# Kernel tuning notes

Measured on AMD Instinct MI355X. Metric: run time of the kernel, lower is better.

## Reference

```python
import jax, jax.numpy as jnp
import numpy as np

B, T, D = 8, 2048, 512
KQ, K = 32, 4  # DemandRouter defaults: k_query=32, k_topk=4


def setup_inputs() -> dict:
    key = jax.random.key(0)
    ks = jax.random.split(key, 9)

    def init(k, shape, fan_in):
        return (jax.random.normal(k, shape, jnp.float32) / np.sqrt(fan_in)).astype(jnp.float32)

    return dict(
        x=jax.random.normal(ks[0], (B, T, D), jnp.float32),
        # DemandRouter projections
        Wq=init(ks[1], (D, KQ), D), bq=jnp.zeros((KQ,), jnp.float32),
        Wk=init(ks[2], (D, KQ), D), bk=jnp.zeros((KQ,), jnp.float32),
        # System1 FFN (D -> 2D -> D) + LayerNorm
        W1=init(ks[3], (D, 2 * D), D), b1=jnp.zeros((2 * D,), jnp.float32),
        W2=init(ks[4], (2 * D, D), 2 * D), b2=jnp.zeros((D,), jnp.float32),
        ln_g=jnp.ones((D,), jnp.float32), ln_b=jnp.zeros((D,), jnp.float32),
        # System2 transform (2D -> 2D -> D)
        Wt1=init(ks[5], (2 * D, 2 * D), 2 * D), bt1=jnp.zeros((2 * D,), jnp.float32),
        Wt2=init(ks[6], (2 * D, D), 2 * D), bt2=jnp.zeros((D,), jnp.float32),
        # output projection
        Wo=init(ks[7], (D, D), D), bo=jnp.zeros((D,), jnp.float32),
    )


def reference(x, Wq, bq, Wk, bk, W1, b1, W2, b2, ln_g, ln_b, Wt1, bt1, Wt2, bt2, Wo, bo):
    # ---- DemandRouter: topk over query-key similarity, gather neighbors, mean ----
    q = x @ Wq + bq                      # [B,T,KQ]
    k = x @ Wk + bk                      # [B,T,KQ]
    sim = jnp.einsum('btk,bsk->bts', q, k) / np.float32(np.sqrt(KQ))  # [B,T,T]
    _, idx = jax.lax.top_k(sim, K)       # [B,T,K]
    # gather x[b, idx[b,t]] and mean over K neighbors -> [B,T,D]
    gathered = jax.vmap(lambda xb, ib: xb[ib])(x, idx).mean(axis=2)

    # ---- System1: residual FFN (exact GELU) + LayerNorm ----
    h = jax.nn.gelu(gathered @ W1 + b1, approximate=False) @ W2 + b2
    y = gathered + h
    mu = y.mean(-1, keepdims=True)
    var = y.var(-1, keepdims=True)
    y = (y - mu) / jnp.sqrt(var + 1e-5) * ln_g + ln_b  # [B,T,D]

    # ---- System2: sequential gated memory update over T ----
    def step(mem, xt):  # mem: [B,D], xt: [B,D]
        e = jnp.concatenate([xt, mem], axis=-1)                       # [B,2D]
        prop = jax.nn.gelu(e @ Wt1 + bt1, approximate=False) @ Wt2 + bt2  # [B,D]
        g = jax.nn.sigmoid(prop)
        mem = mem * (1.0 - g) + prop * g
        return mem, None

    mem0 = jnp.zeros((y.shape[0], y.shape[2]), y.dtype)
    mem_final, _ = jax.lax.scan(step, mem0, jnp.swapaxes(y, 0, 1))

    # pooled = system2_out[:, -1] == final memory
    return mem_final @ Wo + bo  # [B,D]
```

## Files before the change

### kernel.cpp

```cpp
#include <hip/hip_runtime.h>
#include <math.h>
#include <stdint.h>


using bf16x8 = __attribute__((ext_vector_type(8))) short;
using f32x4v = __attribute__((ext_vector_type(4))) float;
typedef unsigned long long ull;

__device__ inline unsigned short f2b(float f) {
  union { float f; unsigned int u; } v; v.f = f;
  unsigned int r = v.u + 0x7fffu + ((v.u >> 16) & 1u);
  return (unsigned short)(r >> 16);
}

__device__ inline float gelu_f(float x) {
  return 0.5f * x * (1.0f + erff(x * 0.70710678118654752f));
}

__device__ inline void ins4(float v, int i,
                            float& v0, int& i0, float& v1, int& i1,
                            float& v2, int& i2, float& v3, int& i3) {
  bool b0 = (v > v0) || (v == v0 && i < i0);
  bool b1 = (v > v1) || (v == v1 && i < i1);
  bool b2 = (v > v2) || (v == v2 && i < i2);
  bool b3 = (v > v3) || (v == v3 && i < i3);
  float nv3 = b2 ? v2 : (b3 ? v : v3); int ni3 = b2 ? i2 : (b3 ? i : i3);
  float nv2 = b1 ? v1 : (b2 ? v : v2); int ni2 = b1 ? i1 : (b2 ? i : i2);
  float nv1 = b0 ? v0 : (b1 ? v : v1); int ni1 = b0 ? i0 : (b1 ? i : i1);
  float nv0 = b0 ? v  : v0;            int ni0 = b0 ? i  : i0;
  v0=nv0; i0=ni0; v1=nv1; i1=ni1; v2=nv2; i2=ni2; v3=nv3; i3=ni3;
}


__global__ __launch_bounds__(256)
void wqk_kernel(const float* __restrict__ Wq, const float* __restrict__ Wk,
                float* __restrict__ wqk) {
  int id = blockIdx.x * 256 + threadIdx.x;
  int d = id >> 6, c = id & 63;
  wqk[id] = (c < 32) ? Wq[d * 32 + c] : Wk[d * 32 + (c - 32)];
}

__global__ __launch_bounds__(256)
void transpose_bf16_kernel(const float* __restrict__ src,
                           unsigned short* __restrict__ dst, int K, int N) {
  __shared__ float tile[32][33];
  int bk = blockIdx.x << 5, bn = blockIdx.y << 5;
  int c = threadIdx.x & 31, r8 = threadIdx.x >> 5;
  for (int r = r8; r < 32; r += 8) tile[r][c] = src[(size_t)(bk + r) * N + bn + c];
  __syncthreads();
  for (int r = r8; r < 32; r += 8) dst[(size_t)(bn + r) * K + bk + c] = f2b(tile[c][r]);
}


__global__ __launch_bounds__(256)
void qk_kernel(const float* __restrict__ x, const float* __restrict__ wqk,
               const float* __restrict__ bq, const float* __restrict__ bk,
               float* __restrict__ qkout) {
  __shared__ float xs[16][512];
  int tid = threadIdx.x;
  int b = blockIdx.x >> 7;
  int t0 = (blockIdx.x & 127) << 4;
  const float* xb = x + ((size_t)(b * 2048 + t0)) * 512;
#pragma unroll
  for (int i = 0; i < 8; ++i) {
    int f = i * 256 + tid;
    int r = f >> 7, c4 = f & 127;
    *(float4*)&xs[r][c4 * 4] = *(const float4*)&xb[(size_t)r * 512 + c4 * 4];
  }
  __syncthreads();
  int c = tid & 63, r4 = tid >> 6;
  float a0 = 0.f, a1 = 0.f, a2 = 0.f, a3 = 0.f;
#pragma unroll 4
  for (int d = 0; d < 512; ++d) {
    float w = wqk[d * 64 + c];
    a0 += xs[r4][d] * w;
    a1 += xs[r4 + 4][d] * w;
    a2 += xs[r4 + 8][d] * w;
    a3 += xs[r4 + 12][d] * w;
  }
  float bias = (c < 32) ? bq[c] : bk[c - 32];
  size_t base = ((size_t)(b * 2048 + t0)) * 64 + c;
  qkout[base + (size_t)r4 * 64] = a0 + bias;
  qkout[base + (size_t)(r4 + 4) * 64] = a1 + bias;
  qkout[base + (size_t)(r4 + 8) * 64] = a2 + bias;
  qkout[base + (size_t)(r4 + 12) * 64] = a3 + bias;
}

__global__ __launch_bounds__(256)
void topk_kernel(const float* __restrict__ qkb, int* __restrict__ idxout) {
  __shared__ float qs[16][36];
  __shared__ float ks[128][36];
  __shared__ float mv[16][16][4];
  __shared__ int   mi[16][16][4];
  int tid = threadIdx.x;
  int b = blockIdx.x >> 7;
  int t0 = (blockIdx.x & 127) << 4;
  const float* qb = qkb + ((size_t)b * 2048) * 64;
  if (tid < 128) {
    int r = tid >> 3, c4 = tid & 7;
    *(float4*)&qs[r][c4 * 4] = *(const float4*)&qb[(size_t)(t0 + r) * 64 + c4 * 4];
  }
  __syncthreads();
  int tl = tid >> 4, sl = tid & 15;
  float qv[32];
#pragma unroll
  for (int kk = 0; kk < 32; ++kk) qv[kk] = qs[tl][kk];
  float v0 = -INFINITY, v1 = -INFINITY, v2 = -INFINITY, v3 = -INFINITY;
  int i0 = 0x7fffffff, i1 = 0x7fffffff, i2 = 0x7fffffff, i3 = 0x7fffffff;
  for (int s0 = 0; s0 < 2048; s0 += 128) {
    __syncthreads();
#pragma unroll
    for (int p = 0; p < 4; ++p) {
      int f = p * 256 + tid;
      int r = f >> 3, c4 = f & 7;
      *(float4*)&ks[r][c4 * 4] =
          *(const float4*)&qb[(size_t)(s0 + r) * 64 + 32 + c4 * 4];
    }
    __syncthreads();
#pragma unroll
    for (int j = 0; j < 8; ++j) {
      int srow = j * 16 + sl;
      float accv = 0.f;
#pragma unroll
      for (int k4 = 0; k4 < 8; ++k4) {
        float4 kv = *(const float4*)&ks[srow][k4 * 4];
        accv += qv[k4 * 4 + 0] * kv.x + qv[k4 * 4 + 1] * kv.y +
                qv[k4 * 4 + 2] * kv.z + qv[k4 * 4 + 3] * kv.w;
      }
      ins4(accv, s0 + srow, v0, i0, v1, i1, v2, i2, v3, i3);
    }
  }
  mv[tl][sl][0] = v0; mv[tl][sl][1] = v1; mv[tl][sl][2] = v2; mv[tl][sl][3] = v3;
  mi[tl][sl][0] = i0; mi[tl][sl][1] = i1; mi[tl][sl][2] = i2; mi[tl][sl][3] = i3;
  __syncthreads();
  if (tid < 16) {
    float w0 = -INFINITY, w1 = -INFINITY, w2 = -INFINITY, w3 = -INFINITY;
    int a0 = 0x7fffffff, a1 = 0x7fffffff, a2 = 0x7fffffff, a3 = 0x7fffffff;
    for (int ss = 0; ss < 16; ++ss)
#pragma unroll
      for (int q = 0; q < 4; ++q)
        ins4(mv[tid][ss][q], mi[tid][ss][q], w0, a0, w1, a1, w2, a2, w3, a3);
    int4 o; o.x = a0; o.y = a1; o.z = a2; o.w = a3;
    *(int4*)&idxout[((size_t)(b * 2048 + t0 + tid)) * 4] = o;
  }
}

__global__ __launch_bounds__(128)
void gather_kernel(const float* __restrict__ x, const int* __restrict__ idx,
                   float* __restrict__ gf, unsigned short* __restrict__ gb) {
  int bt = blockIdx.x;
  int b = bt >> 11;
  const int4 iv = *(const int4*)&idx[(size_t)bt * 4];
  int tid = threadIdx.x;
  const float* xb = x + ((size_t)b * 2048) * 512;
  float4 p0 = *(const float4*)&xb[(size_t)iv.x * 512 + tid * 4];
  float4 p1 = *(const float4*)&xb[(size_t)iv.y * 512 + tid * 4];
  float4 p2 = *(const float4*)&xb[(size_t)iv.z * 512 + tid * 4];
  float4 p3 = *(const float4*)&xb[(size_t)iv.w * 512 + tid * 4];
  float4 m;
  m.x = (p0.x + p1.x + p2.x + p3.x) * 0.25f;
  m.y = (p0.y + p1.y + p2.y + p3.y) * 0.25f;
  m.z = (p0.z + p1.z + p2.z + p3.z) * 0.25f;
  m.w = (p0.w + p1.w + p2.w + p3.w) * 0.25f;
  *(float4*)&gf[(size_t)bt * 512 + tid * 4] = m;
  ushort4 u; u.x = f2b(m.x); u.y = f2b(m.y); u.z = f2b(m.z); u.w = f2b(m.w);
  *(ushort4*)&gb[(size_t)bt * 512 + tid * 4] = u;
}


template <int MODE>
__global__ __launch_bounds__(256, 2)
void gemm_bf16_k(const unsigned short* __restrict__ A,
                 const unsigned short* __restrict__ Bt,
                 const float* __restrict__ bias,
                 const float* __restrict__ resid,
                 void* __restrict__ outp, int M, int N, int K) {
  __shared__ unsigned short sA[128 * 32];
  __shared__ unsigned short sB[128 * 32];
  const int tid = threadIdx.x;
  const int lane = tid & 63, wave = tid >> 6;
  const int m0 = blockIdx.x * 128, n0 = blockIdx.y * 128;
  const int col16 = lane & 15, quad = lane >> 4;
  const int wm = wave >> 1, wn = wave & 1;
  f32x4v acc[4][4];
#pragma unroll
  for (int i = 0; i < 4; ++i)
#pragma unroll
    for (int j = 0; j < 4; ++j) {
      f32x4v z = {0.f, 0.f, 0.f, 0.f};
      acc[i][j] = z;
    }
  const int nkt = K >> 5;
  for (int kt = 0; kt < nkt; ++kt) {
    const int k0 = kt << 5;
#pragma unroll
    for (int p = 0; p < 2; ++p) {
      int f = p * 256 + tid;
      int row = f >> 2, q4 = f & 3;
      *(uint4*)&sA[row * 32 + q4 * 8] =
          *(const uint4*)(A + (size_t)(m0 + row) * K + k0 + q4 * 8);
      *(uint4*)&sB[row * 32 + q4 * 8] =
          *(const uint4*)(Bt + (size_t)(n0 + row) * K + k0 + q4 * 8);
    }
    __syncthreads();
    bf16x8 af[4], bfr[4];
#pragma unroll
    for (int i = 0; i < 4; ++i)
      af[i] = *(const bf16x8*)&sA[(wm * 64 + i * 16 + col16) * 32 + quad * 8];
#pragma unroll
    for (int j = 0; j < 4; ++j)
      bfr[j] = *(const bf16x8*)&sB[(wn * 64 + j * 16 + col16) * 32 + quad * 8];
#pragma unroll
    for (int i = 0; i < 4; ++i)
#pragma unroll
      for (int j = 0; j < 4; ++j)
        acc[i][j] = __builtin_amdgcn_mfma_f32_16x16x32_bf16(af[i], bfr[j],
                                                            acc[i][j], 0, 0, 0);
    __syncthreads();
  }
  float* outf = (float*)outp;
  unsigned short* outb = (unsigned short*)outp;
#pragma unroll
  for (int i = 0; i < 4; ++i)
#pragma unroll
    for (int j = 0; j < 4; ++j) {
      int col = n0 + wn * 64 + j * 16 + col16;
      float bs = bias[col];
#pragma unroll
      for (int r = 0; r < 4; ++r) {
        int row = m0 + wm * 64 + i * 16 + quad * 4 + r;
        float v = acc[i][j][r] + bs;
        if (MODE == 0) {
          outb[(size_t)row * N + col] = f2b(gelu_f(v));
        } else if (MODE == 1) {
          outf[(size_t)row * N + col] = v + resid[(size_t)row * N + col];
        } else {
          outf[(size_t)row * N + col] = v;
        }
      }
    }
}


__global__ __launch_bounds__(128)
void ln_kernel(const float* __restrict__ ypre, const float* __restrict__ lg,
               const float* __restrict__ lb, unsigned short* __restrict__ yb) {
  int row = blockIdx.x, tid = threadIdx.x;
  float4 v = *(const float4*)&ypre[(size_t)row * 512 + tid * 4];
  float s = v.x + v.y + v.z + v.w;
  float sq = v.x * v.x + v.y * v.y + v.z * v.z + v.w * v.w;
#pragma unroll
  for (int off = 1; off < 64; off <<= 1) {
    s += __shfl_xor(s, off, 64);
    sq += __shfl_xor(sq, off, 64);
  }
  __shared__ float red[4];
  if ((tid & 63) == 0) { red[(tid >> 6) * 2] = s; red[(tid >> 6) * 2 + 1] = sq; }
  __syncthreads();
  float S = red[0] + red[2], SQ = red[1] + red[3];
  float mu = S * (1.f / 512.f);
  float var = SQ * (1.f / 512.f) - mu * mu;
  float rstd = rsqrtf(var + 1e-5f);
  float4 g4 = *(const float4*)&lg[tid * 4];
  float4 b4 = *(const float4*)&lb[tid * 4];
  ushort4 u;
  u.x = f2b((v.x - mu) * rstd * g4.x + b4.x);
  u.y = f2b((v.y - mu) * rstd * g4.y + b4.y);
  u.z = f2b((v.z - mu) * rstd * g4.z + b4.z);
  u.w = f2b((v.w - mu) * rstd * g4.w + b4.w);
  *(ushort4*)&yb[(size_t)row * 512 + tid * 4] = u;
}


__global__ __launch_bounds__(256)
void system2_kernel(const float* __restrict__ Wt1, const float* __restrict__ Wt2,
                    const float* __restrict__ bt2, const float* __restrict__ xpart,
                    float* __restrict__ slotbuf, float* __restrict__ membuf,
                    int* __restrict__ flagA, int* __restrict__ flagB,
                    float* __restrict__ memfinal) {
  __shared__ float WbT[32 * 516];
  __shared__ float WtS[32 * 512];
  __shared__ float memS[512];
  __shared__ float parts1[256];
  __shared__ float red2[256];
  __shared__ float guL[32];

  const int t = threadIdx.x;
  const int team = blockIdx.x & 7;
  const int g = blockIdx.x >> 3;
  const int ucol0 = g << 5;
  const int mcol0 = g << 4;

  for (int idx = t; idx < 32 * 512; idx += 256) {
    int j = idx & 31, k = idx >> 5;
    WbT[j * 516 + k] = Wt1[(size_t)(512 + k) * 1024 + ucol0 + j];
  }
  for (int idx = t; idx < 32 * 512; idx += 256) {
    int u = idx >> 9, d = idx & 511;
    WtS[u * 512 + d] = Wt2[(size_t)(ucol0 + u) * 512 + d];
  }
  memS[t] = 0.f;
  memS[t + 256] = 0.f;
  const float bt2r = (t < 16) ? bt2[mcol0 + t] : 0.f;
  __syncthreads();

  const int j = t & 31, c = t >> 5;
  const float* xp = xpart + (size_t)team * 2048 * 1024 + ucol0;
  float xv = (t < 32) ? xp[t] : 0.f;

  for (int s = 0; s < 2048; ++s) {
    const int par = s & 1;
    float* slot = slotbuf + ((size_t)(par * 8 + team) * 32) * 512;
    float* memb = membuf + (size_t)(par * 8 + team) * 512;
    int* flA = flagA + (par * 8 + team) * 32;
    int* flB = flagB + (par * 8 + team) * 32;
    const int tag = s + 1;

    float xnext = (t < 32 && s < 2047) ? xp[(size_t)(s + 1) * 1024 + t] : 0.f;

    {
      const float* wrow = &WbT[j * 516 + c * 64];
      const float* mrow = &memS[c * 64];
      float p1 = 0.f;
#pragma unroll
      for (int i = 0; i < 64; i += 4) {
        float4 wv = *(const float4*)&wrow[i];
        float4 mv = *(const float4*)&mrow[i];
        p1 += wv.x * mv.x + wv.y * mv.y + wv.z * mv.z + wv.w * mv.w;
      }
      parts1[c * 32 + j] = p1;
    }
    __syncthreads();
    if (t < 32) {
      float u = xv;
#pragma unroll
      for (int cc = 0; cc < 8; ++cc) u += parts1[cc * 32 + t];
      guL[t] = gelu_f(u);
    }
    __syncthreads();

    {
      const int d2 = t << 1;
      float px = 0.f, py = 0.f;
#pragma unroll
      for (int u = 0; u < 32; ++u) {
        float gv = guL[u];
        float2 wv = *(const float2*)&WtS[u * 512 + d2];
        px += gv * wv.x;
        py += gv * wv.y;
      }
      union { float2 f2; ull u64; } cv;
      cv.f2 = make_float2(px, py);
      __hip_atomic_store((ull*)&slot[g * 512 + d2], cv.u64, __ATOMIC_RELAXED,
                         __HIP_MEMORY_SCOPE_AGENT);
    }
    __syncthreads();
    if (t == 0)
      __hip_atomic_store(&flA[g], tag, __ATOMIC_RELAXED,
                         __HIP_MEMORY_SCOPE_AGENT);
    if (t < 64) {
      int f = (t < 32) ? 0 : tag;
      const int* fp = &flA[t < 32 ? t : 0];
      while (true) {
        if (t < 32 && f != tag)
          f = __hip_atomic_load(fp, __ATOMIC_RELAXED, __HIP_MEMORY_SCOPE_AGENT);
        if (__ballot(f == tag) == ~0ull) break;
        __builtin_amdgcn_s_sleep(1);
      }
    }
    __syncthreads();
    __builtin_amdgcn_fence(__ATOMIC_ACQUIRE, "workgroup");

    {
      const int w = t >> 4, dd = t & 15;
      float v1 = __hip_atomic_load(&slot[w * 512 + mcol0 + dd], __ATOMIC_RELAXED,
                                   __HIP_MEMORY_SCOPE_AGENT);
      float v2 = __hip_atomic_load(&slot[(w + 16) * 512 + mcol0 + dd],
                                   __ATOMIC_RELAXED, __HIP_MEMORY_SCOPE_AGENT);
      red2[w * 16 + dd] = v1 + v2;
    }
    __syncthreads();
    if (t < 16) {
      float prop = bt2r;
#pragma unroll
      for (int w = 0; w < 16; ++w) prop += red2[w * 16 + t];
      float gate = 1.f / (1.f + __expf(-prop));
      float mnew = memS[mcol0 + t] * (1.f - gate) + prop * gate;
      __hip_atomic_store(&memb[mcol0 + t], mnew, __ATOMIC_RELAXED,
                         __HIP_MEMORY_SCOPE_AGENT);
    }
    __syncthreads();
    if (t == 0)
      __hip_atomic_store(&flB[g], tag, __ATOMIC_RELAXED,
                         __HIP_MEMORY_SCOPE_AGENT);
    if (t < 64) {
      int f = (t < 32) ? 0 : tag;
      const int* fp = &flB[t < 32 ? t : 0];
      while (true) {
        if (t < 32 && f != tag)
          f = __hip_atomic_load(fp, __ATOMIC_RELAXED, __HIP_MEMORY_SCOPE_AGENT);
        if (__ballot(f == tag) == ~0ull) break;
        __builtin_amdgcn_s_sleep(1);
      }
    }
    __syncthreads();
    __builtin_amdgcn_fence(__ATOMIC_ACQUIRE, "workgroup");

    if (t < 128) {
      union { float2 f2; ull u64; } a, b;
      a.u64 = __hip_atomic_load((ull*)&memb[t * 4], __ATOMIC_RELAXED,
                                __HIP_MEMORY_SCOPE_AGENT);
      b.u64 = __hip_atomic_load((ull*)&memb[t * 4 + 2], __ATOMIC_RELAXED,
                                __HIP_MEMORY_SCOPE_AGENT);
      memS[t * 4 + 0] = a.f2.x;
      memS[t * 4 + 1] = a.f2.y;
      memS[t * 4 + 2] = b.f2.x;
      memS[t * 4 + 3] = b.f2.y;
    }
    xv = xnext;
    __syncthreads();
  }

  if (g == 0 && t < 128)
    *(float4*)&memfinal[(size_t)team * 512 + t * 4] = *(float4*)&memS[t * 4];
}


__global__ __launch_bounds__(256)
void out_gemv_kernel(const float* __restrict__ memf, const float* __restrict__ Wo,
                     const float* __restrict__ bo, float* __restrict__ out) {
  int gid = blockIdx.x * 256 + threadIdx.x;
  int b = gid >> 9, d = gid & 511;
  const float* mb = memf + (size_t)b * 512;
  float acc = bo[d];
#pragma unroll 8
  for (int k = 0; k < 512; ++k) acc += mb[k] * Wo[(size_t)k * 512 + d];
  out[gid] = acc;
}


extern "C" void kernel_launch(void* const* d_in, const int* in_sizes, int n_in,
                              void* d_out, int out_size, void* d_ws, size_t ws_size,
                              hipStream_t stream) {
  const float* x   = (const float*)d_in[0];
  const float* Wq  = (const float*)d_in[1];
  const float* bq  = (const float*)d_in[2];
  const float* Wk  = (const float*)d_in[3];
  const float* bk  = (const float*)d_in[4];
  const float* W1  = (const float*)d_in[5];
  const float* b1  = (const float*)d_in[6];
  const float* W2  = (const float*)d_in[7];
  const float* b2  = (const float*)d_in[8];
  const float* lng = (const float*)d_in[9];
  const float* lnb = (const float*)d_in[10];
  const float* Wt1 = (const float*)d_in[11];
  const float* bt1 = (const float*)d_in[12];
  const float* Wt2 = (const float*)d_in[13];
  const float* bt2 = (const float*)d_in[14];
  const float* Wo  = (const float*)d_in[15];
  const float* bo  = (const float*)d_in[16];
  float* out = (float*)d_out;

  char* ws = (char*)d_ws;
  size_t off = 0;
  auto alloc = [&](size_t bytes) -> void* {
    void* p = ws + off;
    off += (bytes + 255) & ~(size_t)255;
    return p;
  };
  float* qk             = (float*)alloc(8ull * 2048 * 64 * 4);
  int* idxb             = (int*)alloc(8ull * 2048 * 4 * 4);
  float* gathf          = (float*)alloc(16384ull * 512 * 4);
  unsigned short* gathb = (unsigned short*)alloc(16384ull * 512 * 2);
  unsigned short* h1b   = (unsigned short*)alloc(16384ull * 1024 * 2);
  float* ypre           = (float*)alloc(16384ull * 512 * 4);
  unsigned short* yb    = (unsigned short*)alloc(16384ull * 512 * 2);
  float* xpart          = (float*)alloc(16384ull * 1024 * 4);
  unsigned short* w1t   = (unsigned short*)alloc(1024ull * 512 * 2);
  unsigned short* w2t   = (unsigned short*)alloc(512ull * 1024 * 2);
  unsigned short* wt1t  = (unsigned short*)alloc(1024ull * 512 * 2);
  float* wqkb           = (float*)alloc(512ull * 64 * 4);
  float* slotbuf        = (float*)alloc(2ull * 8 * 32 * 512 * 4);
  float* membuf         = (float*)alloc(2ull * 8 * 512 * 4);
  int* flagA            = (int*)alloc(2ull * 8 * 32 * 4);
  int* flagB            = (int*)alloc(2ull * 8 * 32 * 4);
  float* memf           = (float*)alloc(8ull * 512 * 4);
  if (off > ws_size) return;

  wqk_kernel<<<128, 256, 0, stream>>>(Wq, Wk, wqkb);
  transpose_bf16_kernel<<<dim3(16, 32), 256, 0, stream>>>(W1, w1t, 512, 1024);
  transpose_bf16_kernel<<<dim3(32, 16), 256, 0, stream>>>(W2, w2t, 1024, 512);
  transpose_bf16_kernel<<<dim3(16, 32), 256, 0, stream>>>(Wt1, wt1t, 512, 1024);

  qk_kernel<<<1024, 256, 0, stream>>>(x, wqkb, bq, bk, qk);
  topk_kernel<<<1024, 256, 0, stream>>>(qk, idxb);
  gather_kernel<<<16384, 128, 0, stream>>>(x, idxb, gathf, gathb);

  gemm_bf16_k<0><<<dim3(128, 8), 256, 0, stream>>>(gathb, w1t, b1, nullptr, h1b,
                                                   16384, 1024, 512);
  gemm_bf16_k<1><<<dim3(128, 4), 256, 0, stream>>>(h1b, w2t, b2, gathf, ypre,
                                                   16384, 512, 1024);
  ln_kernel<<<16384, 128, 0, stream>>>(ypre, lng, lnb, yb);
  gemm_bf16_k<2><<<dim3(128, 8), 256, 0, stream>>>(yb, wt1t, bt1, nullptr, xpart,
                                                   16384, 1024, 512);

  system2_kernel<<<256, 256, 0, stream>>>(Wt1, Wt2, bt2, xpart, slotbuf, membuf,
                                          flagA, flagB, memf);
  out_gemv_kernel<<<16, 256, 0, stream>>>(memf, Wo, bo, out);
}
```

Measured before the change: 8.055 ms.

## Replace flag barriers with tagged 64-bit payloads in system2 cross-block exchange

The sequential scan's cross-block exchange now packs each float together with the step tag into one 64-bit word, so consumers spin directly on the data they need. This removes the separate flag stores, the two __syncthreads around each flag publish, and the ballot-based flag polling. Each step therefore has fewer round trips through global memory. In exchange the exchange buffers double in size and every thread polls global memory, which may add memory traffic. Stale buffers left over from a previous launch could also match a tag if the workspace is not cleared between calls.

```diff
diff --git a/kernel.cpp b/kernel.cpp
--- a/kernel.cpp
+++ b/kernel.cpp
@@ -275,8 +275,7 @@
 __global__ __launch_bounds__(256)
 void system2_kernel(const float* __restrict__ Wt1, const float* __restrict__ Wt2,
                     const float* __restrict__ bt2, const float* __restrict__ xpart,
-                    float* __restrict__ slotbuf, float* __restrict__ membuf,
-                    int* __restrict__ flagA, int* __restrict__ flagB,
+                    ull* __restrict__ slotT, ull* __restrict__ memT,
                     float* __restrict__ memfinal) {
   __shared__ float WbT[32 * 516];
   __shared__ float WtS[32 * 512];
@@ -305,16 +304,16 @@
   __syncthreads();
 
   const int j = t & 31, c = t >> 5;
+  const int w = t >> 4, dd = t & 15;
   const float* xp = xpart + (size_t)team * 2048 * 1024 + ucol0;
   float xv = (t < 32) ? xp[t] : 0.f;
 
   for (int s = 0; s < 2048; ++s) {
     const int par = s & 1;
-    float* slot = slotbuf + ((size_t)(par * 8 + team) * 32) * 512;
-    float* memb = membuf + (size_t)(par * 8 + team) * 512;
-    int* flA = flagA + (par * 8 + team) * 32;
-    int* flB = flagB + (par * 8 + team) * 32;
-    const int tag = s + 1;
+    ull* slot = slotT + ((size_t)(par * 8 + team) * 32) * 512;
+    ull* memb = memT + (size_t)(par * 8 + team) * 512;
+    const unsigned utag = (unsigned)(s + 1);
+    const ull tagw = ((ull)utag) << 32;
 
     float xnext = (t < 32 && s < 2047) ? xp[(size_t)(s + 1) * 1024 + t] : 0.f;
 
@@ -349,73 +348,56 @@
         px += gv * wv.x;
         py += gv * wv.y;
       }
-      union { float2 f2; ull u64; } cv;
-      cv.f2 = make_float2(px, py);
-      __hip_atomic_store((ull*)&slot[g * 512 + d2], cv.u64, __ATOMIC_RELAXED,
+      union { float f; unsigned u; } ax, ay;
+      ax.f = px; ay.f = py;
+      __hip_atomic_store(&slot[g * 512 + d2], tagw | ax.u, __ATOMIC_RELAXED,
                          __HIP_MEMORY_SCOPE_AGENT);
-    }
-    __syncthreads();
-    if (t == 0)
-      __hip_atomic_store(&flA[g], tag, __ATOMIC_RELAXED,
+      __hip_atomic_store(&slot[g * 512 + d2 + 1], tagw | ay.u, __ATOMIC_RELAXED,
                          __HIP_MEMORY_SCOPE_AGENT);
-    if (t < 64) {
-      int f = (t < 32) ? 0 : tag;
-      const int* fp = &flA[t < 32 ? t : 0];
-      while (true) {
-        if (t < 32 && f != tag)
-          f = __hip_atomic_load(fp, __ATOMIC_RELAXED, __HIP_MEMORY_SCOPE_AGENT);
-        if (__ballot(f == tag) == ~0ull) break;
+    }
+    asm volatile("" ::: "memory");
+
+    {
+      ull* p1 = &slot[(size_t)w * 512 + mcol0 + dd];
+      ull* p2 = &slot[(size_t)(w + 16) * 512 + mcol0 + dd];
+      ull v1, v2;
+      for (;;) {
+        v1 = __hip_atomic_load(p1, __ATOMIC_RELAXED, __HIP_MEMORY_SCOPE_AGENT);
+        v2 = __hip_atomic_load(p2, __ATOMIC_RELAXED, __HIP_MEMORY_SCOPE_AGENT);
+        if ((unsigned)(v1 >> 32) == utag && (unsigned)(v2 >> 32) == utag) break;
         __builtin_amdgcn_s_sleep(1);
       }
-    }
-    __syncthreads();
-    __builtin_amdgcn_fence(__ATOMIC_ACQUIRE, "workgroup");
-
-    {
-      const int w = t >> 4, dd = t & 15;
-      float v1 = __hip_atomic_load(&slot[w * 512 + mcol0 + dd], __ATOMIC_RELAXED,
-                                   __HIP_MEMORY_SCOPE_AGENT);
-      float v2 = __hip_atomic_load(&slot[(w + 16) * 512 + mcol0 + dd],
-                                   __ATOMIC_RELAXED, __HIP_MEMORY_SCOPE_AGENT);
-      red2[w * 16 + dd] = v1 + v2;
+      union { unsigned u; float f; } b1, b2;
+      b1.u = (unsigned)v1; b2.u = (unsigned)v2;
+      red2[w * 16 + dd] = b1.f + b2.f;
     }
     __syncthreads();
     if (t < 16) {
       float prop = bt2r;
 #pragma unroll
-      for (int w = 0; w < 16; ++w) prop += red2[w * 16 + t];
+      for (int ww = 0; ww < 16; ++ww) prop += red2[ww * 16 + t];
       float gate = 1.f / (1.f + __expf(-prop));
       float mnew = memS[mcol0 + t] * (1.f - gate) + prop * gate;
-      __hip_atomic_store(&memb[mcol0 + t], mnew, __ATOMIC_RELAXED,
+      union { float f; unsigned u; } mv; mv.f = mnew;
+      __hip_atomic_store(&memb[mcol0 + t], tagw | mv.u, __ATOMIC_RELAXED,
                          __HIP_MEMORY_SCOPE_AGENT);
     }
-    __syncthreads();
-    if (t == 0)
-      __hip_atomic_store(&flB[g], tag, __ATOMIC_RELAXED,
-                         __HIP_MEMORY_SCOPE_AGENT);
-    if (t < 64) {
-      int f = (t < 32) ? 0 : tag;
-      const int* fp = &flB[t < 32 ? t : 0];
-      while (true) {
-        if (t < 32 && f != tag)
-          f = __hip_atomic_load(fp, __ATOMIC_RELAXED, __HIP_MEMORY_SCOPE_AGENT);
-        if (__ballot(f == tag) == ~0ull) break;
+    asm volatile("" ::: "memory");
+
+    {
+      ull* q1 = &memb[t * 2];
+      ull* q2 = &memb[t * 2 + 1];
+      ull v1, v2;
+      for (;;) {
+        v1 = __hip_atomic_load(q1, __ATOMIC_RELAXED, __HIP_MEMORY_SCOPE_AGENT);
+        v2 = __hip_atomic_load(q2, __ATOMIC_RELAXED, __HIP_MEMORY_SCOPE_AGENT);
+        if ((unsigned)(v1 >> 32) == utag && (unsigned)(v2 >> 32) == utag) break;
         __builtin_amdgcn_s_sleep(1);
       }
-    }
-    __syncthreads();
-    __builtin_amdgcn_fence(__ATOMIC_ACQUIRE, "workgroup");
-
-    if (t < 128) {
-      union { float2 f2; ull u64; } a, b;
-      a.u64 = __hip_atomic_load((ull*)&memb[t * 4], __ATOMIC_RELAXED,
-                                __HIP_MEMORY_SCOPE_AGENT);
-      b.u64 = __hip_atomic_load((ull*)&memb[t * 4 + 2], __ATOMIC_RELAXED,
-                                __HIP_MEMORY_SCOPE_AGENT);
-      memS[t * 4 + 0] = a.f2.x;
-      memS[t * 4 + 1] = a.f2.y;
-      memS[t * 4 + 2] = b.f2.x;
-      memS[t * 4 + 3] = b.f2.y;
+      union { unsigned u; float f; } m1, m2;
+      m1.u = (unsigned)v1; m2.u = (unsigned)v2;
+      memS[t * 2] = m1.f;
+      memS[t * 2 + 1] = m2.f;
     }
     xv = xnext;
     __syncthreads();
@@ -480,10 +462,8 @@
   unsigned short* w2t   = (unsigned short*)alloc(512ull * 1024 * 2);
   unsigned short* wt1t  = (unsigned short*)alloc(1024ull * 512 * 2);
   float* wqkb           = (float*)alloc(512ull * 64 * 4);
-  float* slotbuf        = (float*)alloc(2ull * 8 * 32 * 512 * 4);
-  float* membuf         = (float*)alloc(2ull * 8 * 512 * 4);
-  int* flagA            = (int*)alloc(2ull * 8 * 32 * 4);
-  int* flagB            = (int*)alloc(2ull * 8 * 32 * 4);
+  ull* slotT            = (ull*)alloc(2ull * 8 * 32 * 512 * 8);
+  ull* memT             = (ull*)alloc(2ull * 8 * 512 * 8);
   float* memf           = (float*)alloc(8ull * 512 * 4);
   if (off > ws_size) return;
 
@@ -504,7 +484,7 @@
   gemm_bf16_k<2><<<dim3(128, 8), 256, 0, stream>>>(yb, wt1t, bt1, nullptr, xpart,
                                                    16384, 1024, 512);
 
-  system2_kernel<<<256, 256, 0, stream>>>(Wt1, Wt2, bt2, xpart, slotbuf, membuf,
-                                          flagA, flagB, memf);
+  system2_kernel<<<256, 256, 0, stream>>>(Wt1, Wt2, bt2, xpart, slotT, memT,
+                                          memf);
   out_gemv_kernel<<<16, 256, 0, stream>>>(memf, Wo, bo, out);
 }
```

New measurement: 10.25 ms. +27.3%, slower.
